# Optimization experiments

Hardware: AMD Instinct MI355X
Metric: run time of the kernel (lower is better)

## Reference

```python
import jax, jax.numpy as jnp
import numpy as np

N_NODES = 100000


def _gcn_layer(x, src, dst, ew, norm_s, norm_d, W, b):
    # DGL GraphConv with edge weights, norm='both':
    # h_v = D_in(v)^-1/2 * sum_{(u,v) in E} w_uv * D_out(u)^-1/2 * x_u; then Linear.
    m = (x * norm_s[:, None])[src] * ew[:, None]        # [E, d] gather + weight
    agg = jax.ops.segment_sum(m, dst, num_segments=N_NODES)  # [N, d] scatter-add
    return (agg * norm_d[:, None]) @ W + b


def setup_inputs() -> dict:
    key = jax.random.key(0)
    ks = jax.random.split(key, 12)
    N, E, D, C = N_NODES, 1600000, 64, 32
    inp = {
        "x": jax.random.normal(ks[0], (N, D), jnp.float32),
        "src": jax.random.randint(ks[1], (E,), 0, N, jnp.int64),
        "dst": jax.random.randint(ks[2], (E,), 0, N, jnp.int64),
        "ew": jax.random.uniform(ks[3], (E,), jnp.float32),
    }
    s = 1.0 / np.sqrt(D)
    for i, k in zip(range(1, 5), ks[4:8]):
        inp[f"W{i}"] = jax.random.normal(k, (D, D), jnp.float32) * s
        inp[f"b{i}"] = jnp.zeros((D,), jnp.float32)
    inp["Wr"] = jax.random.normal(ks[8], (D, D), jnp.float32) * s
    inp["br"] = jnp.zeros((D,), jnp.float32)
    inp["Wo"] = jax.random.normal(ks[9], (D, C), jnp.float32) * s
    inp["bo"] = jnp.zeros((C,), jnp.float32)
    return inp


def reference(x, src, dst, ew, W1, b1, W2, b2, W3, b3, W4, b4, Wr, br, Wo, bo):
    ones = jnp.ones(src.shape, x.dtype)
    deg_out = jnp.clip(jax.ops.segment_sum(ones, src, num_segments=N_NODES), 1.0)
    deg_in = jnp.clip(jax.ops.segment_sum(ones, dst, num_segments=N_NODES), 1.0)
    norm_s = deg_out ** -0.5
    norm_d = deg_in ** -0.5

    res = x @ Wr + br
    h = jax.nn.relu(_gcn_layer(x, src, dst, ew, norm_s, norm_d, W1, b1))
    h = jax.nn.relu(_gcn_layer(h, src, dst, ew, norm_s, norm_d, W2, b2))
    h = jax.nn.relu(_gcn_layer(h, src, dst, ew, norm_s, norm_d, W3, b3))
    h = _gcn_layer(h, src, dst, ew, norm_s, norm_d, W4, b4)
    h = jax.nn.relu(h + res)
    return h @ Wo + bo
```

## Files before the change

kernel.cpp:

```cpp
#include <hip/hip_runtime.h>

#define NN 100000
#define D 64
#define G 3
#define RS 33334
#define NC 85
#define NB (G*NC)

typedef short bf16x8 __attribute__((ext_vector_type(8)));
typedef float f32x4 __attribute__((ext_vector_type(4)));

__device__ __forceinline__ float bf2f_lo(unsigned w) { return __uint_as_float(w << 16); }
__device__ __forceinline__ float bf2f_hi(unsigned w) { return __uint_as_float(w & 0xffff0000u); }
__device__ __forceinline__ unsigned short f2bf(float f) {
    unsigned u = __float_as_uint(f);
    return (unsigned short)((u + 0x7fffu + ((u >> 16) & 1u)) >> 16);
}
__device__ __forceinline__ unsigned pack2(float a, float b) {
    return (unsigned)f2bf(a) | ((unsigned)f2bf(b) << 16);
}

__global__ __launch_bounds__(1024) void k_hist(const int* __restrict__ src,
                                               const int* __restrict__ dst,
                                               unsigned short* __restrict__ psd, int E) {
    __shared__ unsigned h[RS / 2];
    int b = blockIdx.x, t = threadIdx.x;
    int g = b / NC, c = b - g * NC;
    int lo = g * RS;
    for (int i = t; i < RS / 2; i += 1024) h[i] = 0;
    __syncthreads();
    int e0 = (int)((((long long)c * E / NC)) & ~3LL);
    int e1 = (c == NC - 1) ? E : (int)((((long long)(c + 1) * E / NC)) & ~3LL);
    int m = (e1 - e0) & ~4095;
    for (int e = e0 + t * 4; e < e0 + m; e += 4096) {
        int4 s4 = *(const int4*)(src + e);
        int4 d4 = *(const int4*)(dst + e);
        int v;
        v = s4.x - lo; if ((unsigned)v < RS) atomicAdd(&h[v >> 1], 1u << ((v & 1) * 16));
        v = s4.y - lo; if ((unsigned)v < RS) atomicAdd(&h[v >> 1], 1u << ((v & 1) * 16));
        v = s4.z - lo; if ((unsigned)v < RS) atomicAdd(&h[v >> 1], 1u << ((v & 1) * 16));
        v = s4.w - lo; if ((unsigned)v < RS) atomicAdd(&h[v >> 1], 1u << ((v & 1) * 16));
        v = d4.x - lo; if ((unsigned)v < RS) atomicAdd(&h[v >> 1], 1u << ((v & 1) * 16 + 8));
        v = d4.y - lo; if ((unsigned)v < RS) atomicAdd(&h[v >> 1], 1u << ((v & 1) * 16 + 8));
        v = d4.z - lo; if ((unsigned)v < RS) atomicAdd(&h[v >> 1], 1u << ((v & 1) * 16 + 8));
        v = d4.w - lo; if ((unsigned)v < RS) atomicAdd(&h[v >> 1], 1u << ((v & 1) * 16 + 8));
    }
    for (int e = e0 + m + t; e < e1; e += 1024) {
        int v = src[e] - lo; if ((unsigned)v < RS) atomicAdd(&h[v >> 1], 1u << ((v & 1) * 16));
        v = dst[e] - lo;     if ((unsigned)v < RS) atomicAdd(&h[v >> 1], 1u << ((v & 1) * 16 + 8));
    }
    __syncthreads();
    unsigned* pb = (unsigned*)(psd + (size_t)b * RS);
    for (int i = t; i < RS / 2; i += 1024) pb[i] = h[i];
}

__global__ __launch_bounds__(1024) void k_scan1m(const unsigned short* __restrict__ psd,
                                                 float* __restrict__ ns, float* __restrict__ nd,
                                                 int* __restrict__ rowptr,
                                                 int* __restrict__ bsum, int n) {
    __shared__ int lds[1024];
    int t = threadIdx.x;
    int i = blockIdx.x * 1024 + t;
    int sv = 0, dv = 0;
    if (i < n) {
        int g = i / RS, off = i - g * RS;
        const unsigned short* p = psd + (size_t)(g * NC) * RS + off;
        #pragma unroll 5
        for (int c = 0; c < NC; ++c) {
            unsigned v = p[(size_t)c * RS];
            sv += (int)(v & 0xffu);
            dv += (int)(v >> 8);
        }
        ns[i] = rsqrtf(fmaxf((float)sv, 1.0f));
        nd[i] = rsqrtf(fmaxf((float)dv, 1.0f));
    }
    lds[t] = dv;
    __syncthreads();
    for (int off = 1; off < 1024; off <<= 1) {
        int v = lds[t];
        int a = (t >= off) ? lds[t - off] : 0;
        __syncthreads();
        lds[t] = v + a;
        __syncthreads();
    }
    if (t == 1023) bsum[blockIdx.x] = lds[1023];
    if (i < n) rowptr[i] = lds[t] - dv;
}

__global__ void k_scan3c(int* __restrict__ rowptr, const int* __restrict__ bsum,
                         const unsigned short* __restrict__ psd,
                         unsigned short* __restrict__ cur16,
                         int n, int E, int nb) {
    __shared__ int sbs[128];
    int t = threadIdx.x;
    if (t < 128) sbs[t] = (t < nb) ? bsum[t] : 0;
    __syncthreads();
    for (int off = 1; off < 128; off <<= 1) {
        int v = 0, a = 0;
        if (t < 128) { v = sbs[t]; if (t >= off) a = sbs[t - off]; }
        __syncthreads();
        if (t < 128) sbs[t] = v + a;
        __syncthreads();
    }
    int i = blockIdx.x * blockDim.x + t;
    if (i == 0) rowptr[n] = E;
    if (i >= n) return;
    int blk = i >> 10;
    int base = (blk > 0) ? sbs[blk - 1] : 0;
    int r = rowptr[i] + base;
    rowptr[i] = r;
    int g = i / RS, off = i - g * RS;
    const unsigned short* p = psd + (size_t)(g * NC) * RS + off;
    unsigned short* cp = cur16 + (size_t)(g * NC) * RS + off;
    int run = 0;
    #pragma unroll 5
    for (int c = 0; c < NC; ++c) {
        cp[(size_t)c * RS] = (unsigned short)run;
        run += (int)(p[(size_t)c * RS] >> 8);
    }
}

__global__ __launch_bounds__(1024) void k_fillsort(const int* __restrict__ src,
                                                   const int* __restrict__ dst,
                                                   const float* __restrict__ ew,
                                                   const int* __restrict__ rowptr,
                                                   const unsigned short* __restrict__ cur16,
                                                   int2* __restrict__ cw, int E) {
    __shared__ int cur[RS];
    int b = blockIdx.x, t = threadIdx.x;
    int g = b / NC, c = b - g * NC;
    int lo = g * RS;
    const unsigned short* c16 = cur16 + (size_t)b * RS;
    for (int i = t; i < RS; i += 1024) cur[i] = rowptr[lo + i] + (int)c16[i];
    __syncthreads();
    int e0 = (int)((((long long)c * E / NC)) & ~3LL);
    int e1 = (c == NC - 1) ? E : (int)((((long long)(c + 1) * E / NC)) & ~3LL);
    int m = (e1 - e0) & ~4095;
    for (int e = e0 + t * 4; e < e0 + m; e += 4096) {
        int4 s4 = *(const int4*)(src + e);
        int4 d4 = *(const int4*)(dst + e);
        float4 w4 = *(const float4*)(ew + e);
        int d;
        d = d4.x - lo; if ((unsigned)d < RS) { int p = atomicAdd(&cur[d], 1); cw[p] = make_int2(s4.x, __float_as_int(w4.x)); }
        d = d4.y - lo; if ((unsigned)d < RS) { int p = atomicAdd(&cur[d], 1); cw[p] = make_int2(s4.y, __float_as_int(w4.y)); }
        d = d4.z - lo; if ((unsigned)d < RS) { int p = atomicAdd(&cur[d], 1); cw[p] = make_int2(s4.z, __float_as_int(w4.z)); }
        d = d4.w - lo; if ((unsigned)d < RS) { int p = atomicAdd(&cur[d], 1); cw[p] = make_int2(s4.w, __float_as_int(w4.w)); }
    }
    for (int e = e0 + m + t; e < e1; e += 1024) {
        int d = dst[e] - lo;
        if ((unsigned)d < RS) {
            int p = atomicAdd(&cur[d], 1);
            cw[p] = make_int2(src[e], __float_as_int(ew[e]));
        }
    }
}

__global__ void k_scale(const float* __restrict__ x, const float* __restrict__ ns,
                        unsigned short* __restrict__ xsb, int n16) {
    int i = blockIdx.x * blockDim.x + threadIdx.x;
    if (i < n16) {
        float s = ns[i >> 4];
        float4 v = ((const float4*)x)[i];
        ((uint2*)xsb)[i] = make_uint2(pack2(v.x * s, v.y * s), pack2(v.z * s, v.w * s));
    }
}

template<bool LAST>
__global__ void k_gather(const int* __restrict__ rowptr, const int2* __restrict__ cw,
                         const unsigned short* __restrict__ tmat,
                         const float* __restrict__ nd, const float* __restrict__ ns,
                         const float* __restrict__ bias,
                         const unsigned short* __restrict__ resb,
                         unsigned short* __restrict__ outb, int n, int E) {
    int node = blockIdx.x * (blockDim.x >> 5) + (threadIdx.x >> 5);
    int lane = threadIdx.x & 31;
    if (node >= n) return;
    int g = lane >> 3;
    int h = lane & 7;
    int beg = rowptr[node], end = rowptr[node + 1];
    float a0=0,a1=0,a2=0,a3=0,a4=0,a5=0,a6=0,a7=0;
    float c0=0,c1=0,c2=0,c3=0,c4=0,c5=0,c6=0,c7=0;
    for (int base = beg; base < end; base += 16) {
        int eA = base + g;
        int eB = eA + 4;
        int eC = eA + 8;
        int eD = eA + 12;
        int2 cvA = cw[min(eA, E - 1)];
        int2 cvB = cw[min(eB, E - 1)];
        int2 cvC = cw[min(eC, E - 1)];
        int2 cvD = cw[min(eD, E - 1)];
        float wA = (eA < end) ? __int_as_float(cvA.y) : 0.f;
        float wB = (eB < end) ? __int_as_float(cvB.y) : 0.f;
        float wC = (eC < end) ? __int_as_float(cvC.y) : 0.f;
        float wD = (eD < end) ? __int_as_float(cvD.y) : 0.f;
        uint4 rA = *((const uint4*)(tmat + (size_t)cvA.x * D) + h);
        uint4 rB = *((const uint4*)(tmat + (size_t)cvB.x * D) + h);
        uint4 rC = *((const uint4*)(tmat + (size_t)cvC.x * D) + h);
        uint4 rD = *((const uint4*)(tmat + (size_t)cvD.x * D) + h);
        a0 += wA * bf2f_lo(rA.x); a1 += wA * bf2f_hi(rA.x);
        a2 += wA * bf2f_lo(rA.y); a3 += wA * bf2f_hi(rA.y);
        a4 += wA * bf2f_lo(rA.z); a5 += wA * bf2f_hi(rA.z);
        a6 += wA * bf2f_lo(rA.w); a7 += wA * bf2f_hi(rA.w);
        c0 += wB * bf2f_lo(rB.x); c1 += wB * bf2f_hi(rB.x);
        c2 += wB * bf2f_lo(rB.y); c3 += wB * bf2f_hi(rB.y);
        c4 += wB * bf2f_lo(rB.z); c5 += wB * bf2f_hi(rB.z);
        c6 += wB * bf2f_lo(rB.w); c7 += wB * bf2f_hi(rB.w);
        a0 += wC * bf2f_lo(rC.x); a1 += wC * bf2f_hi(rC.x);
        a2 += wC * bf2f_lo(rC.y); a3 += wC * bf2f_hi(rC.y);
        a4 += wC * bf2f_lo(rC.z); a5 += wC * bf2f_hi(rC.z);
        a6 += wC * bf2f_lo(rC.w); a7 += wC * bf2f_hi(rC.w);
        c0 += wD * bf2f_lo(rD.x); c1 += wD * bf2f_hi(rD.x);
        c2 += wD * bf2f_lo(rD.y); c3 += wD * bf2f_hi(rD.y);
        c4 += wD * bf2f_lo(rD.z); c5 += wD * bf2f_hi(rD.z);
        c6 += wD * bf2f_lo(rD.w); c7 += wD * bf2f_hi(rD.w);
    }
    a0 += c0; a1 += c1; a2 += c2; a3 += c3;
    a4 += c4; a5 += c5; a6 += c6; a7 += c7;
    #pragma unroll
    for (int msk = 8; msk <= 16; msk <<= 1) {
        a0 += __shfl_xor(a0, msk); a1 += __shfl_xor(a1, msk);
        a2 += __shfl_xor(a2, msk); a3 += __shfl_xor(a3, msk);
        a4 += __shfl_xor(a4, msk); a5 += __shfl_xor(a5, msk);
        a6 += __shfl_xor(a6, msk); a7 += __shfl_xor(a7, msk);
    }
    float ndv = nd[node];
    float4 b0 = *(const float4*)(bias + 8 * h);
    float4 b1 = *(const float4*)(bias + 8 * h + 4);
    float v0 = ndv * a0 + b0.x, v1 = ndv * a1 + b0.y;
    float v2 = ndv * a2 + b0.z, v3 = ndv * a3 + b0.w;
    float v4 = ndv * a4 + b1.x, v5 = ndv * a5 + b1.y;
    float v6 = ndv * a6 + b1.z, v7 = ndv * a7 + b1.w;
    if (LAST) {
        uint4 r = *((const uint4*)(resb + (size_t)node * D) + h);
        v0 += bf2f_lo(r.x); v1 += bf2f_hi(r.x);
        v2 += bf2f_lo(r.y); v3 += bf2f_hi(r.y);
        v4 += bf2f_lo(r.z); v5 += bf2f_hi(r.z);
        v6 += bf2f_lo(r.w); v7 += bf2f_hi(r.w);
    }
    v0 = fmaxf(v0, 0.f); v1 = fmaxf(v1, 0.f); v2 = fmaxf(v2, 0.f); v3 = fmaxf(v3, 0.f);
    v4 = fmaxf(v4, 0.f); v5 = fmaxf(v5, 0.f); v6 = fmaxf(v6, 0.f); v7 = fmaxf(v7, 0.f);
    if (!LAST) {
        float s = ns[node];
        v0 *= s; v1 *= s; v2 *= s; v3 *= s; v4 *= s; v5 *= s; v6 *= s; v7 *= s;
    }
    if (g == 0) {
        uint4 o = make_uint4(pack2(v0, v1), pack2(v2, v3), pack2(v4, v5), pack2(v6, v7));
        *((uint4*)(outb + (size_t)node * D) + h) = o;
    }
}

template<int OUTD, bool BIAS, bool IN_BF16, bool OUT_BF16>
__global__ __launch_bounds__(256) void k_gemm(const void* __restrict__ in_,
                                              const float* __restrict__ W,
                                              const float* __restrict__ bias,
                                              void* __restrict__ out_, int n) {
    constexpr int NT = OUTD / 16;
    __shared__ unsigned short WT[OUTD][72];
    int t = threadIdx.x;
    for (int i = t; i < 64 * OUTD; i += 256) {
        int k = i / OUTD, nn = i % OUTD;
        WT[nn][k] = f2bf(W[i]);
    }
    __syncthreads();
    int w = t >> 6, lane = t & 63;
    int m = lane & 15, q = lane >> 4;
    int node0 = blockIdx.x * 64 + w * 16;
    int nodeA = min(node0 + m, n - 1);
    bf16x8 afr[2];
    if (IN_BF16) {
        const unsigned short* inb = (const unsigned short*)in_ + (size_t)nodeA * D;
        #pragma unroll
        for (int kc = 0; kc < 2; ++kc) {
            union { bf16x8 v; uint4 u; } tmp;
            tmp.u = *(const uint4*)(inb + kc * 32 + q * 8);
            afr[kc] = tmp.v;
        }
    } else {
        const float* inf = (const float*)in_ + (size_t)nodeA * D;
        #pragma unroll
        for (int kc = 0; kc < 2; ++kc) {
            float4 f0 = *(const float4*)(inf + kc * 32 + q * 8);
            float4 f1 = *(const float4*)(inf + kc * 32 + q * 8 + 4);
            union { bf16x8 v; unsigned short u[8]; } tmp;
            tmp.u[0] = f2bf(f0.x); tmp.u[1] = f2bf(f0.y);
            tmp.u[2] = f2bf(f0.z); tmp.u[3] = f2bf(f0.w);
            tmp.u[4] = f2bf(f1.x); tmp.u[5] = f2bf(f1.y);
            tmp.u[6] = f2bf(f1.z); tmp.u[7] = f2bf(f1.w);
            afr[kc] = tmp.v;
        }
    }
    #pragma unroll
    for (int nt = 0; nt < NT; ++nt) {
        f32x4 acc = {0.f, 0.f, 0.f, 0.f};
        #pragma unroll
        for (int kc = 0; kc < 2; ++kc) {
            union { bf16x8 v; uint4 u; } bfr;
            bfr.u = *(const uint4*)&WT[nt * 16 + m][kc * 32 + q * 8];
            acc = __builtin_amdgcn_mfma_f32_16x16x32_bf16(afr[kc], bfr.v, acc, 0, 0, 0);
        }
        int col = nt * 16 + m;
        float bb = BIAS ? bias[col] : 0.f;
        #pragma unroll
        for (int r = 0; r < 4; ++r) {
            int node = node0 + q * 4 + r;
            if (node < n) {
                float v = acc[r] + bb;
                if (OUT_BF16)
                    ((unsigned short*)out_)[(size_t)node * OUTD + col] = f2bf(v);
                else
                    ((float*)out_)[(size_t)node * OUTD + col] = v;
            }
        }
    }
}

static inline char* align_up(char* p, size_t a) {
    return (char*)(((uintptr_t)p + a - 1) & ~(uintptr_t)(a - 1));
}

extern "C" void kernel_launch(void* const* d_in, const int* in_sizes, int n_in,
                              void* d_out, int out_size, void* d_ws, size_t ws_size,
                              hipStream_t stream) {
    const float* x   = (const float*)d_in[0];
    const int*   src = (const int*)d_in[1];
    const int*   dst = (const int*)d_in[2];
    const float* ew  = (const float*)d_in[3];
    const float* Wl[4] = {(const float*)d_in[4], (const float*)d_in[6],
                          (const float*)d_in[8], (const float*)d_in[10]};
    const float* bl[4] = {(const float*)d_in[5], (const float*)d_in[7],
                          (const float*)d_in[9], (const float*)d_in[11]};
    const float* Wr = (const float*)d_in[12];
    const float* br = (const float*)d_in[13];
    const float* Wo = (const float*)d_in[14];
    const float* bo = (const float*)d_in[15];
    float* out = (float*)d_out;

    const int N = NN;
    const int E = in_sizes[1];

    char* p = (char*)d_ws;
    float* norm_s = (float*)p;            p = align_up(p + N * 4, 256);
    float* norm_d = (float*)p;            p = align_up(p + N * 4, 256);
    int*   rowptr = (int*)p;              p = align_up(p + (size_t)(G * RS + 80) * 4, 256);
    int*   bsum   = (int*)p;              p = align_up(p + 128 * 4, 256);
    int2*  cw     = (int2*)p;             p = align_up(p + (size_t)E * 8, 256);
    unsigned short* psd   = (unsigned short*)p; p = align_up(p + (size_t)NB * RS * 2, 256);
    unsigned short* cur16 = (unsigned short*)p; p = align_up(p + (size_t)NB * RS * 2, 256);
    unsigned short* resb  = (unsigned short*)p; p = align_up(p + (size_t)N * D * 2, 256);
    unsigned short* xs   = psd;
    unsigned short* tmat = xs + (size_t)N * D;

    k_hist<<<NB, 1024, 0, stream>>>(src, dst, psd, E);
    int nb = (N + 1023) / 1024;
    k_scan1m<<<nb, 1024, 0, stream>>>(psd, norm_s, norm_d, rowptr, bsum, N);
    k_scan3c<<<(N + 255) / 256, 256, 0, stream>>>(rowptr, bsum, psd, cur16, N, E, nb);
    k_fillsort<<<NB, 1024, 0, stream>>>(src, dst, ew, rowptr, cur16, cw, E);

    k_scale<<<(N * 16 + 255) / 256, 256, 0, stream>>>(x, norm_s, xs, N * 16);
    k_gemm<64, true, false, true><<<(N + 63) / 64, 256, 0, stream>>>(x, Wr, br, resb, N);

    for (int l = 0; l < 4; ++l) {
        k_gemm<64, false, true, true><<<(N + 63) / 64, 256, 0, stream>>>(
            xs, Wl[l], nullptr, tmat, N);
        if (l < 3) {
            k_gather<false><<<(N + 7) / 8, 256, 0, stream>>>(
                rowptr, cw, tmat, norm_d, norm_s, bl[l], nullptr, xs, N, E);
        } else {
            k_gather<true><<<(N + 7) / 8, 256, 0, stream>>>(
                rowptr, cw, tmat, norm_d, nullptr, bl[l], resb, xs, N, E);
        }
    }
    k_gemm<32, true, true, false><<<(N + 63) / 64, 256, 0, stream>>>(xs, Wo, bo, out, N);
}
```

Measured before the change: 357.9 us.

## Split gather feature dimension into two halves across separate blocks

The gather kernel now gives each node's 64 features to two 32-lane groups in different blocks, each handling a 32-feature half with 8-byte loads. Blocks are ordered so that the two halves of a 32-node group are scheduled close together, which should raise parallelism and cut per-thread register use. The cost is that every edge's index and weight are read twice and each row fetch now moves 64 bytes instead of 128, which may use memory transactions less efficiently.

After: 454.6 us. 1.27x slower.

```diff
diff --git a/kernel.cpp b/kernel.cpp
--- a/kernel.cpp
+++ b/kernel.cpp
@@ -172,14 +172,19 @@
                          const float* __restrict__ bias,
                          const unsigned short* __restrict__ resb,
                          unsigned short* __restrict__ outb, int n, int E) {
-    int node = blockIdx.x * (blockDim.x >> 5) + (threadIdx.x >> 5);
+    int b = blockIdx.x;
+    int grp = b >> 3, r = b & 7;
+    int half = r >> 2, sub = r & 3;
+    int hw = threadIdx.x >> 5;
+    int node = grp * 32 + sub * 8 + hw;
     int lane = threadIdx.x & 31;
     if (node >= n) return;
     int g = lane >> 3;
     int h = lane & 7;
+    const unsigned short* tb = tmat + half * 32;
     int beg = rowptr[node], end = rowptr[node + 1];
-    float a0=0,a1=0,a2=0,a3=0,a4=0,a5=0,a6=0,a7=0;
-    float c0=0,c1=0,c2=0,c3=0,c4=0,c5=0,c6=0,c7=0;
+    float a0=0,a1=0,a2=0,a3=0;
+    float c0=0,c1=0,c2=0,c3=0;
     for (int base = beg; base < end; base += 16) {
         int eA = base + g;
         int eB = eA + 4;
@@ -193,59 +198,43 @@
         float wB = (eB < end) ? __int_as_float(cvB.y) : 0.f;
         float wC = (eC < end) ? __int_as_float(cvC.y) : 0.f;
         float wD = (eD < end) ? __int_as_float(cvD.y) : 0.f;
-        uint4 rA = *((const uint4*)(tmat + (size_t)cvA.x * D) + h);
-        uint4 rB = *((const uint4*)(tmat + (size_t)cvB.x * D) + h);
-        uint4 rC = *((const uint4*)(tmat + (size_t)cvC.x * D) + h);
-        uint4 rD = *((const uint4*)(tmat + (size_t)cvD.x * D) + h);
+        uint2 rA = *((const uint2*)(tb + (size_t)cvA.x * D) + h);
+        uint2 rB = *((const uint2*)(tb + (size_t)cvB.x * D) + h);
+        uint2 rC = *((const uint2*)(tb + (size_t)cvC.x * D) + h);
+        uint2 rD = *((const uint2*)(tb + (size_t)cvD.x * D) + h);
         a0 += wA * bf2f_lo(rA.x); a1 += wA * bf2f_hi(rA.x);
         a2 += wA * bf2f_lo(rA.y); a3 += wA * bf2f_hi(rA.y);
-        a4 += wA * bf2f_lo(rA.z); a5 += wA * bf2f_hi(rA.z);
-        a6 += wA * bf2f_lo(rA.w); a7 += wA * bf2f_hi(rA.w);
         c0 += wB * bf2f_lo(rB.x); c1 += wB * bf2f_hi(rB.x);
         c2 += wB * bf2f_lo(rB.y); c3 += wB * bf2f_hi(rB.y);
-        c4 += wB * bf2f_lo(rB.z); c5 += wB * bf2f_hi(rB.z);
-        c6 += wB * bf2f_lo(rB.w); c7 += wB * bf2f_hi(rB.w);
         a0 += wC * bf2f_lo(rC.x); a1 += wC * bf2f_hi(rC.x);
         a2 += wC * bf2f_lo(rC.y); a3 += wC * bf2f_hi(rC.y);
-        a4 += wC * bf2f_lo(rC.z); a5 += wC * bf2f_hi(rC.z);
-        a6 += wC * bf2f_lo(rC.w); a7 += wC * bf2f_hi(rC.w);
         c0 += wD * bf2f_lo(rD.x); c1 += wD * bf2f_hi(rD.x);
         c2 += wD * bf2f_lo(rD.y); c3 += wD * bf2f_hi(rD.y);
-        c4 += wD * bf2f_lo(rD.z); c5 += wD * bf2f_hi(rD.z);
-        c6 += wD * bf2f_lo(rD.w); c7 += wD * bf2f_hi(rD.w);
     }
     a0 += c0; a1 += c1; a2 += c2; a3 += c3;
-    a4 += c4; a5 += c5; a6 += c6; a7 += c7;
     #pragma unroll
     for (int msk = 8; msk <= 16; msk <<= 1) {
         a0 += __shfl_xor(a0, msk); a1 += __shfl_xor(a1, msk);
         a2 += __shfl_xor(a2, msk); a3 += __shfl_xor(a3, msk);
-        a4 += __shfl_xor(a4, msk); a5 += __shfl_xor(a5, msk);
-        a6 += __shfl_xor(a6, msk); a7 += __shfl_xor(a7, msk);
     }
     float ndv = nd[node];
-    float4 b0 = *(const float4*)(bias + 8 * h);
-    float4 b1 = *(const float4*)(bias + 8 * h + 4);
-    float v0 = ndv * a0 + b0.x, v1 = ndv * a1 + b0.y;
-    float v2 = ndv * a2 + b0.z, v3 = ndv * a3 + b0.w;
-    float v4 = ndv * a4 + b1.x, v5 = ndv * a5 + b1.y;
-    float v6 = ndv * a6 + b1.z, v7 = ndv * a7 + b1.w;
+    int fo = half * 32 + 4 * h;
+    float4 bb = *(const float4*)(bias + fo);
+    float v0 = ndv * a0 + bb.x, v1 = ndv * a1 + bb.y;
+    float v2 = ndv * a2 + bb.z, v3 = ndv * a3 + bb.w;
     if (LAST) {
-        uint4 r = *((const uint4*)(resb + (size_t)node * D) + h);
-        v0 += bf2f_lo(r.x); v1 += bf2f_hi(r.x);
-        v2 += bf2f_lo(r.y); v3 += bf2f_hi(r.y);
-        v4 += bf2f_lo(r.z); v5 += bf2f_hi(r.z);
-        v6 += bf2f_lo(r.w); v7 += bf2f_hi(r.w);
+        uint2 rr = *((const uint2*)(resb + (size_t)node * D + half * 32) + h);
+        v0 += bf2f_lo(rr.x); v1 += bf2f_hi(rr.x);
+        v2 += bf2f_lo(rr.y); v3 += bf2f_hi(rr.y);
     }
     v0 = fmaxf(v0, 0.f); v1 = fmaxf(v1, 0.f); v2 = fmaxf(v2, 0.f); v3 = fmaxf(v3, 0.f);
-    v4 = fmaxf(v4, 0.f); v5 = fmaxf(v5, 0.f); v6 = fmaxf(v6, 0.f); v7 = fmaxf(v7, 0.f);
     if (!LAST) {
         float s = ns[node];
-        v0 *= s; v1 *= s; v2 *= s; v3 *= s; v4 *= s; v5 *= s; v6 *= s; v7 *= s;
+        v0 *= s; v1 *= s; v2 *= s; v3 *= s;
     }
     if (g == 0) {
-        uint4 o = make_uint4(pack2(v0, v1), pack2(v2, v3), pack2(v4, v5), pack2(v6, v7));
-        *((uint4*)(outb + (size_t)node * D) + h) = o;
+        *((uint2*)(outb + (size_t)node * D + half * 32) + h) =
+            make_uint2(pack2(v0, v1), pack2(v2, v3));
     }
 }
 
@@ -359,14 +348,15 @@
     k_scale<<<(N * 16 + 255) / 256, 256, 0, stream>>>(x, norm_s, xs, N * 16);
     k_gemm<64, true, false, true><<<(N + 63) / 64, 256, 0, stream>>>(x, Wr, br, resb, N);
 
+    int ggrid = ((N + 31) / 32) * 8;
     for (int l = 0; l < 4; ++l) {
         k_gemm<64, false, true, true><<<(N + 63) / 64, 256, 0, stream>>>(
             xs, Wl[l], nullptr, tmat, N);
         if (l < 3) {
-            k_gather<false><<<(N + 7) / 8, 256, 0, stream>>>(
+            k_gather<false><<<ggrid, 256, 0, stream>>>(
                 rowptr, cw, tmat, norm_d, norm_s, bl[l], nullptr, xs, N, E);
         } else {
-            k_gather<true><<<(N + 7) / 8, 256, 0, stream>>>(
+            k_gather<true><<<ggrid, 256, 0, stream>>>(
                 rowptr, cw, tmat, norm_d, nullptr, bl[l], resb, xs, N, E);
         }
     }
```
